# Performance work log

Hardware: AMD Instinct MI355X
Metric: run time of the kernel (lower is better)

The kernel has to match this reference:

```python
import jax, jax.numpy as jnp
import numpy as np

NUM_HEADS = 16


def setup_inputs() -> dict:
    key = jax.random.key(0)
    ks = jax.random.split(key, 7)
    E = 1024
    s = 0.02
    return {
        "x": jax.random.normal(ks[0], (2, 2048, E), dtype=jnp.float32),
        "Wq": jax.random.normal(ks[1], (E, E), dtype=jnp.float32) * s,
        "bq": jax.random.normal(ks[2], (E,), dtype=jnp.float32) * s,
        "Wk": jax.random.normal(ks[3], (E, E), dtype=jnp.float32) * s,
        "bk": jax.random.normal(ks[4], (E,), dtype=jnp.float32) * s,
        "Wv": jax.random.normal(ks[5], (E, E), dtype=jnp.float32) * s,
        "bv": jax.random.normal(ks[6], (E,), dtype=jnp.float32) * s,
    }


def reference(x, Wq, bq, Wk, bk, Wv, bv):
    b, s, e = x.shape
    h = NUM_HEADS
    d = e // h  # head_dim = 64
    # nn.Linear: y = x @ W^T + b
    q = x @ Wq.T + bq
    k = x @ Wk.T + bk
    v = x @ Wv.T + bv
    # Faithful reshape chain from the source: (b,s,e)->(b,s,h,d)->(-1,s,d)
    # (raw reshape, NO transpose, matching the original buggy layout)
    q = q.reshape(b, s, h, d).reshape(-1, s, d)
    k = k.reshape(b, s, h, d).reshape(-1, s, d)
    v = v.reshape(b, s, h, d).reshape(-1, s, d)
    # Scaled scores; note the source returns qk @ v (softmax result discarded)
    scale = 1.0 / np.sqrt(d).astype(np.float32)
    qk = jnp.einsum('bqd,bkd->bqk', q, k) * scale  # [b*h, s, s]
    out = jnp.einsum('bqk,bkd->bqd', qk, v)        # [b*h, s, d]
    return out
```

## Files before the change

### kernel.cpp

```cpp
#include <hip/hip_runtime.h>
#include <hip/hip_bf16.h>


#define E_DIM 1024
#define N_ROWS 4096

typedef __attribute__((ext_vector_type(8))) short bf16x8;
typedef __attribute__((ext_vector_type(4))) float f32x4;

#define QB_U 0
#define KB_U 4194304
#define VB_U 8388608
#define XB_U 12582912
#define WB_U 16777216
#define P_F  9961472
#define TB_U 24117248

__device__ __forceinline__ unsigned short f2b(float f) {
    union { float f; unsigned int i; } c; c.f = f;
    unsigned int r = c.i + 0x7FFFu + ((c.i >> 16) & 1u);
    return (unsigned short)(r >> 16);
}

typedef __attribute__((address_space(1))) const void* gptr_t;
typedef __attribute__((address_space(3))) void* lptr_t;
__device__ __forceinline__ void gl_lds16(const void* g, void* l) {
    __builtin_amdgcn_global_load_lds((gptr_t)g, (lptr_t)l, 16, 0, 0);
}

__global__ __launch_bounds__(256) void cvt_bf16(
    const float* __restrict__ x,  const float* __restrict__ wq,
    const float* __restrict__ wk, const float* __restrict__ wv,
    unsigned short* __restrict__ dst0)
{
    const int seg = blockIdx.y;
    const float* __restrict__ src;
    unsigned short* __restrict__ dst;
    if (seg < 4) { src = x + (size_t)seg * 1048576; dst = dst0 + (size_t)seg * 1048576; }
    else {
        src = (seg == 4) ? wq : (seg == 5) ? wk : wv;
        dst = dst0 + 4194304 + (size_t)(seg - 4) * 1048576;
    }
    const int i = blockIdx.x * 256 + threadIdx.x;
    const float4 a = *(const float4*)(src + (size_t)i * 8);
    const float4 b = *(const float4*)(src + (size_t)i * 8 + 4);
    uint4 o;
    o.x = (unsigned)f2b(a.x) | ((unsigned)f2b(a.y) << 16);
    o.y = (unsigned)f2b(a.z) | ((unsigned)f2b(a.w) << 16);
    o.z = (unsigned)f2b(b.x) | ((unsigned)f2b(b.y) << 16);
    o.w = (unsigned)f2b(b.z) | ((unsigned)f2b(b.w) << 16);
    *(uint4*)(dst + (size_t)i * 8) = o;
}

__global__ __launch_bounds__(256, 3) void qkv_gemm_mfma(
    const unsigned short* __restrict__ Xb,
    const unsigned short* __restrict__ Wb,
    const float* __restrict__ bq, const float* __restrict__ bk,
    const float* __restrict__ bv,
    unsigned short* __restrict__ qkv)
{
    const int which = blockIdx.z;
    const unsigned short* __restrict__ W = Wb + (size_t)which * (1024 * 1024);
    const float* __restrict__ bias = (which == 0) ? bq : (which == 1) ? bk : bv;
    unsigned short* __restrict__ Y = qkv + (size_t)which * ((size_t)N_ROWS * E_DIM);

    __shared__ __align__(16) unsigned short Als[128 * 32];
    __shared__ __align__(16) unsigned short Bls[128 * 32];

    const int tid  = threadIdx.x;
    const int w    = tid >> 6;
    const int lane = tid & 63;
    const int m0 = blockIdx.x * 128;
    const int n0 = blockIdx.y * 128;
    const int wm = (w >> 1) * 64;
    const int wn = (w & 1) * 64;

    f32x4 acc[4][4];
    #pragma unroll
    for (int i = 0; i < 4; ++i)
        #pragma unroll
        for (int j = 0; j < 4; ++j)
            acc[i][j] = f32x4{0.f, 0.f, 0.f, 0.f};

    const int srow = w * 32 + (lane >> 2);
    const int skc  = (lane & 3) * 8;
    const int kq   = (lane >> 4) * 8;
    const int fm   = lane & 15;

    for (int k0 = 0; k0 < E_DIM; k0 += 32) {
        gl_lds16((const void*)(Xb + (size_t)(m0 + srow) * E_DIM + k0 + skc),
                 (void*)((char*)Als + (w * 2 + 0) * 1024));
        gl_lds16((const void*)(Xb + (size_t)(m0 + srow + 16) * E_DIM + k0 + skc),
                 (void*)((char*)Als + (w * 2 + 1) * 1024));
        gl_lds16((const void*)(W + (size_t)(n0 + srow) * E_DIM + k0 + skc),
                 (void*)((char*)Bls + (w * 2 + 0) * 1024));
        gl_lds16((const void*)(W + (size_t)(n0 + srow + 16) * E_DIM + k0 + skc),
                 (void*)((char*)Bls + (w * 2 + 1) * 1024));
        __syncthreads();

        bf16x8 af[4], bf[4];
        #pragma unroll
        for (int t = 0; t < 4; ++t) {
            af[t] = *(const bf16x8*)(Als + (wm + t * 16 + fm) * 32 + kq);
            bf[t] = *(const bf16x8*)(Bls + (wn + t * 16 + fm) * 32 + kq);
        }
        #pragma unroll
        for (int rt = 0; rt < 4; ++rt)
            #pragma unroll
            for (int ct = 0; ct < 4; ++ct)
                acc[rt][ct] = __builtin_amdgcn_mfma_f32_16x16x32_bf16(
                    af[rt], bf[ct], acc[rt][ct], 0, 0, 0);
        __syncthreads();
    }

    float bcol[4];
    #pragma unroll
    for (int ct = 0; ct < 4; ++ct) bcol[ct] = bias[n0 + wn + ct * 16 + fm];

    const int rbase = (lane >> 4) * 4;
    #pragma unroll
    for (int rt = 0; rt < 4; ++rt) {
        #pragma unroll
        for (int ct = 0; ct < 4; ++ct) {
            #pragma unroll
            for (int r = 0; r < 4; ++r) {
                const int row = m0 + wm + rt * 16 + rbase + r;
                const int col = n0 + wn + ct * 16 + fm;
                Y[(size_t)row * E_DIM + col] = f2b(acc[rt][ct][r] + bcol[ct]);
            }
        }
    }
}

__global__ __launch_bounds__(256) void kT_mfma(
    const unsigned short* __restrict__ qkv, float* __restrict__ P)
{
    const size_t base = (size_t)blockIdx.x * (2048 * 64) + (size_t)blockIdx.y * (128 * 64);
    const unsigned short* __restrict__ Kb = qkv + KB_U + base;
    const unsigned short* __restrict__ Vb = qkv + VB_U + base;
    float* __restrict__ Pout = P + ((size_t)blockIdx.x * 16 + blockIdx.y) * 4096;

    __shared__ __align__(16) unsigned short Kt[64 * 64];
    __shared__ __align__(16) unsigned short Vt[64 * 64];

    const int tid  = threadIdx.x;
    const int w    = tid >> 6;
    const int lane = tid & 63;
    const int rl   = tid & 63;
    const int eo   = (tid >> 6) * 16;
    const int kq   = (lane >> 4) * 8;
    const int fm   = lane & 15;

    f32x4 acc[4];
    #pragma unroll
    for (int nt = 0; nt < 4; ++nt) acc[nt] = f32x4{0.f, 0.f, 0.f, 0.f};

    for (int rb = 0; rb < 128; rb += 64) {
        union { uint4 u; unsigned short s[8]; } k0, k1, v0, v1;
        const size_t ga = (size_t)(rb + rl) * 64 + eo;
        k0.u = *(const uint4*)(Kb + ga);
        k1.u = *(const uint4*)(Kb + ga + 8);
        v0.u = *(const uint4*)(Vb + ga);
        v1.u = *(const uint4*)(Vb + ga + 8);
        __syncthreads();
        #pragma unroll
        for (int j = 0; j < 8; ++j) {
            Kt[(eo + j) * 64 + rl]     = k0.s[j];
            Kt[(eo + 8 + j) * 64 + rl] = k1.s[j];
            Vt[(eo + j) * 64 + rl]     = v0.s[j];
            Vt[(eo + 8 + j) * 64 + rl] = v1.s[j];
        }
        __syncthreads();
        #pragma unroll
        for (int kk = 0; kk < 2; ++kk) {
            const bf16x8 af = *(const bf16x8*)(Vt + (w * 16 + fm) * 64 + kk * 32 + kq);
            #pragma unroll
            for (int nt = 0; nt < 4; ++nt) {
                const bf16x8 bf = *(const bf16x8*)(Kt + (nt * 16 + fm) * 64 + kk * 32 + kq);
                acc[nt] = __builtin_amdgcn_mfma_f32_16x16x32_bf16(af, bf, acc[nt], 0, 0, 0);
            }
        }
    }

    const int rbase = (lane >> 4) * 4;
    #pragma unroll
    for (int nt = 0; nt < 4; ++nt)
        #pragma unroll
        for (int r = 0; r < 4; ++r)
            Pout[(size_t)(w * 16 + rbase + r) * 64 + nt * 16 + fm] = acc[nt][r];
}

__global__ __launch_bounds__(256) void reduce_T(
    const float* __restrict__ P, unsigned short* __restrict__ TB)
{
    const int idx = blockIdx.x * 256 + threadIdx.x;
    const int i   = idx >> 12;
    const int off = idx & 4095;
    const float* p = P + (size_t)i * 16 * 4096 + off;
    float s = 0.0f;
    #pragma unroll
    for (int c = 0; c < 16; ++c) s += p[(size_t)c * 4096];
    TB[(size_t)i * 4096 + off] = f2b(s);
}

__global__ __launch_bounds__(256, 2) void qT_mfma(
    const unsigned short* __restrict__ qkv,
    const unsigned short* __restrict__ TB,
    float* __restrict__ out)
{
    __shared__ __align__(16) unsigned short Als[128 * 64];
    __shared__ __align__(16) unsigned short Bls[64 * 64];

    const int bx   = blockIdx.x;
    const int r0   = bx * 128;
    const int i    = bx >> 4;
    const int tid  = threadIdx.x;
    const int w    = tid >> 6;
    const int lane = tid & 63;
    const int kq   = (lane >> 4) * 8;
    const int fm   = lane & 15;

    const unsigned short* __restrict__ Qb = qkv + QB_U + (size_t)r0 * 64;
    const unsigned short* __restrict__ Tb = TB + (size_t)i * 4096;

    #pragma unroll
    for (int c = 0; c < 4; ++c)
        gl_lds16((const void*)(Qb + (w * 4 + c) * 512 + lane * 8),
                 (void*)((char*)Als + (w * 4 + c) * 1024));
    #pragma unroll
    for (int c = 0; c < 2; ++c)
        gl_lds16((const void*)(Tb + (w * 2 + c) * 512 + lane * 8),
                 (void*)((char*)Bls + (w * 2 + c) * 1024));
    __syncthreads();

    bf16x8 af[2][2], bf[4][2];
    #pragma unroll
    for (int mt = 0; mt < 2; ++mt)
        #pragma unroll
        for (int kk = 0; kk < 2; ++kk)
            af[mt][kk] = *(const bf16x8*)(Als + (w * 32 + mt * 16 + fm) * 64 + kk * 32 + kq);
    #pragma unroll
    for (int nt = 0; nt < 4; ++nt)
        #pragma unroll
        for (int kk = 0; kk < 2; ++kk)
            bf[nt][kk] = *(const bf16x8*)(Bls + (nt * 16 + fm) * 64 + kk * 32 + kq);

    f32x4 acc[2][4];
    #pragma unroll
    for (int mt = 0; mt < 2; ++mt)
        #pragma unroll
        for (int nt = 0; nt < 4; ++nt)
            acc[mt][nt] = f32x4{0.f, 0.f, 0.f, 0.f};

    #pragma unroll
    for (int kk = 0; kk < 2; ++kk)
        #pragma unroll
        for (int mt = 0; mt < 2; ++mt)
            #pragma unroll
            for (int nt = 0; nt < 4; ++nt)
                acc[mt][nt] = __builtin_amdgcn_mfma_f32_16x16x32_bf16(
                    af[mt][kk], bf[nt][kk], acc[mt][nt], 0, 0, 0);

    const int rbase = (lane >> 4) * 4;
    #pragma unroll
    for (int mt = 0; mt < 2; ++mt) {
        #pragma unroll
        for (int nt = 0; nt < 4; ++nt) {
            #pragma unroll
            for (int r = 0; r < 4; ++r) {
                const int row = r0 + w * 32 + mt * 16 + rbase + r;
                const int col = nt * 16 + fm;
                out[(size_t)row * 64 + col] = 0.125f * acc[mt][nt][r];
            }
        }
    }
}

extern "C" void kernel_launch(void* const* d_in, const int* in_sizes, int n_in,
                              void* d_out, int out_size, void* d_ws, size_t ws_size,
                              hipStream_t stream)
{
    const float* x  = (const float*)d_in[0];
    const float* Wq = (const float*)d_in[1];
    const float* bq = (const float*)d_in[2];
    const float* Wk = (const float*)d_in[3];
    const float* bk = (const float*)d_in[4];
    const float* Wv = (const float*)d_in[5];
    const float* bv = (const float*)d_in[6];
    float* wsf = (float*)d_ws;
    unsigned short* wsu = (unsigned short*)d_ws;
    float* out = (float*)d_out;

    dim3 gCvt(512, 7);
    cvt_bf16<<<gCvt, 256, 0, stream>>>(x, Wq, Wk, Wv, wsu + XB_U);

    dim3 gA(N_ROWS / 128, E_DIM / 128, 3);
    qkv_gemm_mfma<<<gA, 256, 0, stream>>>(wsu + XB_U, wsu + WB_U,
                                          bq, bk, bv, wsu + QB_U);

    dim3 gB(32, 16);
    kT_mfma<<<gB, 256, 0, stream>>>(wsu, wsf + P_F);

    reduce_T<<<512, 256, 0, stream>>>(wsf + P_F, wsu + TB_U);

    qT_mfma<<<512, 256, 0, stream>>>(wsu, wsu + TB_U, out);
}
```

Measured before the change: 130.5 us.

## XOR-swizzle LDS tiles in all MFMA kernels and halve kT split count

Applies XOR swizzling to the shared-memory layouts of the QKV GEMM, the K^T V kernel and the Q·T kernel, so fragment reads and transposed writes spread across LDS banks instead of conflicting. It also makes each kT block process 256 rows instead of 128, halving the partial-sum buffers and the reduction work in reduce_T. The trade-off is more index arithmetic and fewer kT blocks, which lowers parallelism in that stage.

```diff
diff --git a/kernel.cpp b/kernel.cpp
--- a/kernel.cpp
+++ b/kernel.cpp
@@ -83,9 +83,10 @@
             acc[i][j] = f32x4{0.f, 0.f, 0.f, 0.f};
 
     const int srow = w * 32 + (lane >> 2);
-    const int skc  = (lane & 3) * 8;
-    const int kq   = (lane >> 4) * 8;
+    const int skc  = ((lane & 3) ^ ((lane >> 3) & 3)) * 8;
+    const int quad = lane >> 4;
     const int fm   = lane & 15;
+    const int sw2  = (fm >> 1) & 3;
 
     for (int k0 = 0; k0 < E_DIM; k0 += 32) {
         gl_lds16((const void*)(Xb + (size_t)(m0 + srow) * E_DIM + k0 + skc),
@@ -98,11 +99,12 @@
                  (void*)((char*)Bls + (w * 2 + 1) * 1024));
         __syncthreads();
 
+        const int slot = (quad ^ sw2) * 8;
         bf16x8 af[4], bf[4];
         #pragma unroll
         for (int t = 0; t < 4; ++t) {
-            af[t] = *(const bf16x8*)(Als + (wm + t * 16 + fm) * 32 + kq);
-            bf[t] = *(const bf16x8*)(Bls + (wn + t * 16 + fm) * 32 + kq);
+            af[t] = *(const bf16x8*)(Als + (wm + t * 16 + fm) * 32 + slot);
+            bf[t] = *(const bf16x8*)(Bls + (wn + t * 16 + fm) * 32 + slot);
         }
         #pragma unroll
         for (int rt = 0; rt < 4; ++rt)
@@ -132,13 +134,17 @@
     }
 }
 
+__device__ __forceinline__ int sw_idx(int row, int r) {
+    return row * 64 + (((((r) >> 3) & 7) ^ (row & 7)) << 3) + (r & 7);
+}
+
 __global__ __launch_bounds__(256) void kT_mfma(
     const unsigned short* __restrict__ qkv, float* __restrict__ P)
 {
-    const size_t base = (size_t)blockIdx.x * (2048 * 64) + (size_t)blockIdx.y * (128 * 64);
+    const size_t base = (size_t)blockIdx.x * (2048 * 64) + (size_t)blockIdx.y * (256 * 64);
     const unsigned short* __restrict__ Kb = qkv + KB_U + base;
     const unsigned short* __restrict__ Vb = qkv + VB_U + base;
-    float* __restrict__ Pout = P + ((size_t)blockIdx.x * 16 + blockIdx.y) * 4096;
+    float* __restrict__ Pout = P + ((size_t)blockIdx.x * 8 + blockIdx.y) * 4096;
 
     __shared__ __align__(16) unsigned short Kt[64 * 64];
     __shared__ __align__(16) unsigned short Vt[64 * 64];
@@ -148,14 +154,15 @@
     const int lane = tid & 63;
     const int rl   = tid & 63;
     const int eo   = (tid >> 6) * 16;
-    const int kq   = (lane >> 4) * 8;
+    const int quad = lane >> 4;
     const int fm   = lane & 15;
+    const int sw8  = fm & 7;
 
     f32x4 acc[4];
     #pragma unroll
     for (int nt = 0; nt < 4; ++nt) acc[nt] = f32x4{0.f, 0.f, 0.f, 0.f};
 
-    for (int rb = 0; rb < 128; rb += 64) {
+    for (int rb = 0; rb < 256; rb += 64) {
         union { uint4 u; unsigned short s[8]; } k0, k1, v0, v1;
         const size_t ga = (size_t)(rb + rl) * 64 + eo;
         k0.u = *(const uint4*)(Kb + ga);
@@ -165,18 +172,19 @@
         __syncthreads();
         #pragma unroll
         for (int j = 0; j < 8; ++j) {
-            Kt[(eo + j) * 64 + rl]     = k0.s[j];
-            Kt[(eo + 8 + j) * 64 + rl] = k1.s[j];
-            Vt[(eo + j) * 64 + rl]     = v0.s[j];
-            Vt[(eo + 8 + j) * 64 + rl] = v1.s[j];
+            Kt[sw_idx(eo + j, rl)]     = k0.s[j];
+            Kt[sw_idx(eo + 8 + j, rl)] = k1.s[j];
+            Vt[sw_idx(eo + j, rl)]     = v0.s[j];
+            Vt[sw_idx(eo + 8 + j, rl)] = v1.s[j];
         }
         __syncthreads();
         #pragma unroll
         for (int kk = 0; kk < 2; ++kk) {
-            const bf16x8 af = *(const bf16x8*)(Vt + (w * 16 + fm) * 64 + kk * 32 + kq);
+            const int slot = ((kk * 4 + quad) ^ sw8) << 3;
+            const bf16x8 af = *(const bf16x8*)(Vt + (w * 16 + fm) * 64 + slot);
             #pragma unroll
             for (int nt = 0; nt < 4; ++nt) {
-                const bf16x8 bf = *(const bf16x8*)(Kt + (nt * 16 + fm) * 64 + kk * 32 + kq);
+                const bf16x8 bf = *(const bf16x8*)(Kt + (nt * 16 + fm) * 64 + slot);
                 acc[nt] = __builtin_amdgcn_mfma_f32_16x16x32_bf16(af, bf, acc[nt], 0, 0, 0);
             }
         }
@@ -196,10 +204,10 @@
     const int idx = blockIdx.x * 256 + threadIdx.x;
     const int i   = idx >> 12;
     const int off = idx & 4095;
-    const float* p = P + (size_t)i * 16 * 4096 + off;
+    const float* p = P + (size_t)i * 8 * 4096 + off;
     float s = 0.0f;
     #pragma unroll
-    for (int c = 0; c < 16; ++c) s += p[(size_t)c * 4096];
+    for (int c = 0; c < 8; ++c) s += p[(size_t)c * 4096];
     TB[(size_t)i * 4096 + off] = f2b(s);
 }
 
@@ -217,19 +225,21 @@
     const int tid  = threadIdx.x;
     const int w    = tid >> 6;
     const int lane = tid & 63;
-    const int kq   = (lane >> 4) * 8;
+    const int quad = lane >> 4;
     const int fm   = lane & 15;
+    const int sw8  = fm & 7;
 
     const unsigned short* __restrict__ Qb = qkv + QB_U + (size_t)r0 * 64;
     const unsigned short* __restrict__ Tb = TB + (size_t)i * 4096;
 
+    const int soff = (lane >> 3) * 64 + (((lane & 7) ^ ((lane >> 3) & 7)) << 3);
     #pragma unroll
     for (int c = 0; c < 4; ++c)
-        gl_lds16((const void*)(Qb + (w * 4 + c) * 512 + lane * 8),
+        gl_lds16((const void*)(Qb + (w * 4 + c) * 512 + soff),
                  (void*)((char*)Als + (w * 4 + c) * 1024));
     #pragma unroll
     for (int c = 0; c < 2; ++c)
-        gl_lds16((const void*)(Tb + (w * 2 + c) * 512 + lane * 8),
+        gl_lds16((const void*)(Tb + (w * 2 + c) * 512 + soff),
                  (void*)((char*)Bls + (w * 2 + c) * 1024));
     __syncthreads();
 
@@ -238,12 +248,14 @@
     for (int mt = 0; mt < 2; ++mt)
         #pragma unroll
         for (int kk = 0; kk < 2; ++kk)
-            af[mt][kk] = *(const bf16x8*)(Als + (w * 32 + mt * 16 + fm) * 64 + kk * 32 + kq);
+            af[mt][kk] = *(const bf16x8*)(Als + (w * 32 + mt * 16 + fm) * 64
+                                          + (((kk * 4 + quad) ^ sw8) << 3));
     #pragma unroll
     for (int nt = 0; nt < 4; ++nt)
         #pragma unroll
         for (int kk = 0; kk < 2; ++kk)
-            bf[nt][kk] = *(const bf16x8*)(Bls + (nt * 16 + fm) * 64 + kk * 32 + kq);
+            bf[nt][kk] = *(const bf16x8*)(Bls + (nt * 16 + fm) * 64
+                                          + (((kk * 4 + quad) ^ sw8) << 3));
 
     f32x4 acc[2][4];
     #pragma unroll
@@ -298,7 +310,7 @@
     qkv_gemm_mfma<<<gA, 256, 0, stream>>>(wsu + XB_U, wsu + WB_U,
                                           bq, bk, bv, wsu + QB_U);
 
-    dim3 gB(32, 16);
+    dim3 gB(32, 8);
     kT_mfma<<<gB, 256, 0, stream>>>(wsu, wsf + P_F);
 
     reduce_T<<<512, 256, 0, stream>>>(wsf + P_F, wsu + TB_U);
```

After: 130.1 us. About the same (-0.3%).
